# Kernel optimization log

Measured on AMD Instinct MI355X. Metric: run time of the kernel, lower is better.

Reference implementation:

```python
import jax, jax.numpy as jnp
import numpy as np

GAMMA = 0.95        # gamma_lemma: persistence decay per cycle (eq. 12.1)
KAPPA = 0.1         # kappa_interfere: lateral interference strength (eq. 12.3)
T_STEPS = 50        # t_lemma_steps: integration window before selection (eq. 12.2)
FLOOR = 1e-6        # confidence_floor for peak-to-average ratio

B, N_CONCEPTS, N_LEMMAS = 4096, 1024, 512


def setup_inputs() -> dict:
    key = jax.random.key(0)
    k1, k2 = jax.random.split(key, 2)
    # kernel boundary hands in a normalized concept distribution
    c_raw = jax.random.uniform(k1, (B, N_CONCEPTS), dtype=jnp.float32)
    c_lex = c_raw / jnp.sum(c_raw, axis=-1, keepdims=True)
    # TiedSubstrate W_C_to_L: (out_dim=n_lemmas, in_dim=n_concepts)
    W = jax.random.normal(k2, (N_LEMMAS, N_CONCEPTS), dtype=jnp.float32) / np.sqrt(N_CONCEPTS)
    # persistent lemma activation buffer a_lemma, zero at reset
    a0 = jnp.zeros((B, N_LEMMAS), dtype=jnp.float32)
    return {"c_lex": c_lex, "W": W, "a0": a0}


def reference(c_lex, W, a0):
    """Integrate lemma activations for T_STEPS cycles, then select.

    Per cycle (eq. 12.1 + 12.3):
      a <- gamma * a + c_lex @ W^T            # decay + concept->lemma drive
      a <- a - kappa * (sum_j a_j - a)        # lateral interference from other lemmas
      a <- max(a, 0)                          # rectify activations
    Selection (eq. 12.2): argmax over lemmas; confidence = peak / max(mean, floor).
    """
    def step(a, _):
        a = GAMMA * a + jnp.einsum('bc,lc->bl', c_lex, W)   # (B, n_lemmas)
        a = a - KAPPA * (jnp.sum(a, axis=-1, keepdims=True) - a)
        a = jnp.maximum(a, 0.0)
        return a, None

    a, _ = jax.lax.scan(step, a0, None, length=T_STEPS)
    peak = jnp.max(a, axis=-1)
    mean = jnp.mean(a, axis=-1)
    confidence = peak / jnp.maximum(mean, FLOOR)
    selected = jnp.argmax(a, axis=-1)
    return a, selected, confidence
```

## Files before the change

kernel.cpp:

```cpp
#include <hip/hip_runtime.h>
#include <hip/hip_bf16.h>

#define BATCH 4096
#define NC    1024
#define NL    512
#define TSTEPS 50
#define GAMMA_C 0.95f
#define KAPPA_C 0.1f
#define FLOOR_C 1e-6f

typedef __attribute__((ext_vector_type(8))) short short8;
typedef __attribute__((ext_vector_type(4))) float f32x4;

__device__ inline void split_bf16(float x, unsigned short& h, unsigned short& l) {
    unsigned u = __float_as_uint(x);
    unsigned rh = u + 0x7FFFu + ((u >> 16) & 1u);
    h = (unsigned short)(rh >> 16);
    float hf = __uint_as_float((unsigned)h << 16);
    float r = x - hf;
    unsigned v = __float_as_uint(r);
    unsigned rl = v + 0x7FFFu + ((v >> 16) & 1u);
    l = (unsigned short)(rl >> 16);
}

__global__ __launch_bounds__(256)
void convert_split(const float* __restrict__ A, const float* __restrict__ W,
                   unsigned short* __restrict__ Ahi, unsigned short* __restrict__ Alo,
                   unsigned short* __restrict__ Whi, unsigned short* __restrict__ Wlo) {
    const int chunk = blockIdx.x * 256 + threadIdx.x;
    const int fidx  = chunk * 4;
    const float* src;
    unsigned short *dh, *dl;
    if (fidx < BATCH * NC) {
        src = A + fidx; dh = Ahi + fidx; dl = Alo + fidx;
    } else {
        const int o = fidx - BATCH * NC;
        src = W + o; dh = Whi + o; dl = Wlo + o;
    }
    const float4 v = *(const float4*)src;
    ushort4 h4, l4;
    split_bf16(v.x, h4.x, l4.x);
    split_bf16(v.y, h4.y, l4.y);
    split_bf16(v.z, h4.z, l4.z);
    split_bf16(v.w, h4.w, l4.w);
    *(ushort4*)dh = h4;
    *(ushort4*)dl = l4;
}

#define TM 128
#define TN 256
#define GK 32
#define LDT 40

__global__ __launch_bounds__(512)
void gemm_bf16x2(const unsigned short* __restrict__ Ahi, const unsigned short* __restrict__ Alo,
                 const unsigned short* __restrict__ Whi, const unsigned short* __restrict__ Wlo,
                 float* __restrict__ Dp, int kPerSplit) {
    __shared__ unsigned short AsH[TM * LDT];
    __shared__ unsigned short AsL[TM * LDT];
    __shared__ unsigned short BsH[TN * LDT];
    __shared__ unsigned short BsL[TN * LDT];

    const int tid = threadIdx.x;
    const int m0 = blockIdx.x * TM;
    const int n0 = blockIdx.y * TN;
    const int kb = blockIdx.z * kPerSplit;

    const int srA = tid >> 2;
    const int kcA = (tid & 3) * 8;
    const int srB = tid >> 1;
    const int kcB = (tid & 1) * 16;

    const unsigned short* gAh = Ahi + (size_t)(m0 + srA) * NC + kb + kcA;
    const unsigned short* gAl = Alo + (size_t)(m0 + srA) * NC + kb + kcA;
    const unsigned short* gBh = Whi + (size_t)(n0 + srB) * NC + kb + kcB;
    const unsigned short* gBl = Wlo + (size_t)(n0 + srB) * NC + kb + kcB;

    unsigned short* wAh = AsH + srA * LDT + kcA;
    unsigned short* wAl = AsL + srA * LDT + kcA;
    unsigned short* wBh = BsH + srB * LDT + kcB;
    unsigned short* wBl = BsL + srB * LDT + kcB;

    const int lane = tid & 63;
    const int w    = tid >> 6;
    const int mw   = (w >> 2) * 64;
    const int nw   = (w & 3) * 64;
    const int sr   = lane & 15;
    const int quad = lane >> 4;

    const unsigned short* rAh = AsH + (mw + sr) * LDT + quad * 8;
    const unsigned short* rAl = AsL + (mw + sr) * LDT + quad * 8;
    const unsigned short* rBh = BsH + (nw + sr) * LDT + quad * 8;
    const unsigned short* rBl = BsL + (nw + sr) * LDT + quad * 8;

    f32x4 acc[4][4];
    #pragma unroll
    for (int i = 0; i < 4; ++i)
        #pragma unroll
        for (int j = 0; j < 4; ++j)
            acc[i][j] = (f32x4){0.f, 0.f, 0.f, 0.f};

    short8 pAh = *(const short8*)gAh;
    short8 pAl = *(const short8*)gAl;
    short8 pBh0 = *(const short8*)gBh;
    short8 pBh1 = *(const short8*)(gBh + 8);
    short8 pBl0 = *(const short8*)gBl;
    short8 pBl1 = *(const short8*)(gBl + 8);

    for (int kt = 0; kt < kPerSplit; kt += GK) {
        *(short8*)wAh = pAh;
        *(short8*)wAl = pAl;
        *(short8*)wBh = pBh0;
        *(short8*)(wBh + 8) = pBh1;
        *(short8*)wBl = pBl0;
        *(short8*)(wBl + 8) = pBl1;
        __syncthreads();

        const int kn = (kt + GK < kPerSplit) ? kt + GK : 0;
        pAh = *(const short8*)(gAh + kn);
        pAl = *(const short8*)(gAl + kn);
        pBh0 = *(const short8*)(gBh + kn);
        pBh1 = *(const short8*)(gBh + kn + 8);
        pBl0 = *(const short8*)(gBl + kn);
        pBl1 = *(const short8*)(gBl + kn + 8);

        short8 afh[4], afl[4], bfh[4], bfl[4];
        #pragma unroll
        for (int mi = 0; mi < 4; ++mi) {
            afh[mi] = *(const short8*)(rAh + mi * 16 * LDT);
            afl[mi] = *(const short8*)(rAl + mi * 16 * LDT);
        }
        #pragma unroll
        for (int ni = 0; ni < 4; ++ni) {
            bfh[ni] = *(const short8*)(rBh + ni * 16 * LDT);
            bfl[ni] = *(const short8*)(rBl + ni * 16 * LDT);
        }

        #pragma unroll
        for (int mi = 0; mi < 4; ++mi) {
            #pragma unroll
            for (int ni = 0; ni < 4; ++ni) {
                acc[mi][ni] = __builtin_amdgcn_mfma_f32_16x16x32_bf16(
                    afh[mi], bfh[ni], acc[mi][ni], 0, 0, 0);
                acc[mi][ni] = __builtin_amdgcn_mfma_f32_16x16x32_bf16(
                    afh[mi], bfl[ni], acc[mi][ni], 0, 0, 0);
                acc[mi][ni] = __builtin_amdgcn_mfma_f32_16x16x32_bf16(
                    afl[mi], bfh[ni], acc[mi][ni], 0, 0, 0);
            }
        }
        __syncthreads();
    }

    float* Dz = Dp + (size_t)blockIdx.z * BATCH * NL;
    #pragma unroll
    for (int mi = 0; mi < 4; ++mi) {
        #pragma unroll
        for (int ni = 0; ni < 4; ++ni) {
            const int col = n0 + nw + ni * 16 + sr;
            #pragma unroll
            for (int r = 0; r < 4; ++r) {
                const int row = m0 + mw + mi * 16 + quad * 4 + r;
                Dz[(size_t)row * NL + col] = acc[mi][ni][r];
            }
        }
    }
}

template<int SK>
__global__ __launch_bounds__(256)
void iterate_select(const float* __restrict__ Dp,
                    float* __restrict__ a_out,
                    float* __restrict__ sel_out, float* __restrict__ conf_out) {
    const int lane = threadIdx.x & 63;
    const int wave = threadIdx.x >> 6;
    const int sub  = lane & 31;
    const int grp  = lane >> 5;
    const int row  = blockIdx.x * 8 + wave * 2 + grp;

    float d[16];
    {
        const float4* p0 = (const float4*)(Dp + (size_t)row * NL + sub * 16);
        #pragma unroll
        for (int p = 0; p < 4; ++p) {
            const float4 v = p0[p];
            d[4 * p + 0] = v.x; d[4 * p + 1] = v.y; d[4 * p + 2] = v.z; d[4 * p + 3] = v.w;
        }
        #pragma unroll
        for (int s = 1; s < SK; ++s) {
            const float4* ps = (const float4*)(Dp + (size_t)s * BATCH * NL
                                               + (size_t)row * NL + sub * 16);
            #pragma unroll
            for (int p = 0; p < 4; ++p) {
                const float4 v = ps[p];
                d[4 * p + 0] += v.x; d[4 * p + 1] += v.y;
                d[4 * p + 2] += v.z; d[4 * p + 3] += v.w;
            }
        }
    }

    float a[16];
    #pragma unroll
    for (int j = 0; j < 16; ++j) a[j] = 0.f;

    const float K1 = 1.0f + KAPPA_C;

    for (int t = 0; t < TSTEPS; ++t) {
        #pragma unroll
        for (int j = 0; j < 16; ++j) a[j] = fmaf(GAMMA_C, a[j], d[j]);

        float t8[8], t4[4], t2[2];
        #pragma unroll
        for (int j = 0; j < 8; ++j) t8[j] = a[j] + a[j + 8];
        #pragma unroll
        for (int j = 0; j < 4; ++j) t4[j] = t8[j] + t8[j + 4];
        t2[0] = t4[0] + t4[2]; t2[1] = t4[1] + t4[3];
        float S = t2[0] + t2[1];

        S += __shfl_xor(S, 1, 64);
        S += __shfl_xor(S, 2, 64);
        S += __shfl_xor(S, 4, 64);
        S += __shfl_xor(S, 8, 64);
        S += __shfl_xor(S, 16, 64);

        const float h = -KAPPA_C * S;
        #pragma unroll
        for (int j = 0; j < 16; ++j) {
            const float v = fmaf(K1, a[j], h);
            a[j] = v > 0.f ? v : 0.f;
        }
    }

    float m8[8], m4[4], s8[8], s4[4];
    #pragma unroll
    for (int j = 0; j < 8; ++j) { m8[j] = fmaxf(a[j], a[j + 8]); s8[j] = a[j] + a[j + 8]; }
    #pragma unroll
    for (int j = 0; j < 4; ++j) { m4[j] = fmaxf(m8[j], m8[j + 4]); s4[j] = s8[j] + s8[j + 4]; }
    float peak = fmaxf(fmaxf(m4[0], m4[1]), fmaxf(m4[2], m4[3]));
    float ssum = (s4[0] + s4[1]) + (s4[2] + s4[3]);

    peak = fmaxf(peak, __shfl_xor(peak, 1, 64));
    peak = fmaxf(peak, __shfl_xor(peak, 2, 64));
    peak = fmaxf(peak, __shfl_xor(peak, 4, 64));
    peak = fmaxf(peak, __shfl_xor(peak, 8, 64));
    peak = fmaxf(peak, __shfl_xor(peak, 16, 64));
    ssum += __shfl_xor(ssum, 1, 64);
    ssum += __shfl_xor(ssum, 2, 64);
    ssum += __shfl_xor(ssum, 4, 64);
    ssum += __shfl_xor(ssum, 8, 64);
    ssum += __shfl_xor(ssum, 16, 64);

    const float mean = ssum * (1.0f / (float)NL);
    const float conf = peak / fmaxf(mean, FLOOR_C);

    int idx = 0x7fffffff;
    #pragma unroll
    for (int j = 0; j < 16; ++j)
        if (a[j] == peak) idx = min(idx, sub * 16 + j);
    idx = min(idx, __shfl_xor(idx, 1, 64));
    idx = min(idx, __shfl_xor(idx, 2, 64));
    idx = min(idx, __shfl_xor(idx, 4, 64));
    idx = min(idx, __shfl_xor(idx, 8, 64));
    idx = min(idx, __shfl_xor(idx, 16, 64));

    float4* ar = (float4*)(a_out + (size_t)row * NL + sub * 16);
    #pragma unroll
    for (int p = 0; p < 4; ++p) {
        float4 v;
        v.x = a[4 * p + 0]; v.y = a[4 * p + 1]; v.z = a[4 * p + 2]; v.w = a[4 * p + 3];
        ar[p] = v;
    }

    if (sub == 0) {
        if (sel_out)  sel_out[row]  = (float)idx;
        if (conf_out) conf_out[row] = conf;
    }
}

extern "C" void kernel_launch(void* const* d_in, const int* in_sizes, int n_in,
                              void* d_out, int out_size, void* d_ws, size_t ws_size,
                              hipStream_t stream) {
    const float* c_lex = (const float*)d_in[0];
    const float* W     = (const float*)d_in[1];

    float* D = (float*)d_ws;
    unsigned short* Ahi = (unsigned short*)(D + 4ull * BATCH * NL);
    unsigned short* Alo = Ahi + (size_t)BATCH * NC;
    unsigned short* Whi = Alo + (size_t)BATCH * NC;
    unsigned short* Wlo = Whi + (size_t)NL * NC;

    float* a_out = (float*)d_out;
    float* sel   = nullptr;
    float* conf  = nullptr;
    const int base = BATCH * NL;
    if (out_size >= base + 2 * BATCH) {
        sel  = a_out + base;
        conf = a_out + base + BATCH;
    } else if (out_size >= base + BATCH) {
        conf = a_out + base;
    }

    convert_split<<<dim3(4608), 256, 0, stream>>>(c_lex, W, Ahi, Alo, Whi, Wlo);

    const int kPerSplit = NC / 4;
    gemm_bf16x2<<<dim3(BATCH / TM, NL / TN, 4), 512, 0, stream>>>(
        Ahi, Alo, Whi, Wlo, D, kPerSplit);

    iterate_select<4><<<dim3(BATCH / 8), 256, 0, stream>>>(D, a_out, sel, conf);
}
```

Measured before the change: 115.1 us.

## Fuse activation bf16 split into GEMM load and widen iterate rows to full wave

Removes the separate conversion pass over the concept activations: the GEMM now loads fp32 A tiles directly and splits them into hi/lo bf16 in registers before writing to shared memory, so only W is pre-split. This avoids writing and re-reading the two bf16 copies of A (about 16MB of traffic) at the cost of more conversion ALU work in the GEMM's store phase. The iterate kernel also switches from two rows per wave with 16 elements per lane to one row per wave with 8 elements per lane, which doubles the block count and adds one shuffle stage per reduction.

After: 113.4 us. About the same (-1.5%).

```diff
diff --git a/kernel.cpp b/kernel.cpp
--- a/kernel.cpp
+++ b/kernel.cpp
@@ -24,27 +24,17 @@
 }
 
 __global__ __launch_bounds__(256)
-void convert_split(const float* __restrict__ A, const float* __restrict__ W,
-                   unsigned short* __restrict__ Ahi, unsigned short* __restrict__ Alo,
-                   unsigned short* __restrict__ Whi, unsigned short* __restrict__ Wlo) {
-    const int chunk = blockIdx.x * 256 + threadIdx.x;
-    const int fidx  = chunk * 4;
-    const float* src;
-    unsigned short *dh, *dl;
-    if (fidx < BATCH * NC) {
-        src = A + fidx; dh = Ahi + fidx; dl = Alo + fidx;
-    } else {
-        const int o = fidx - BATCH * NC;
-        src = W + o; dh = Whi + o; dl = Wlo + o;
-    }
-    const float4 v = *(const float4*)src;
+void convert_w(const float* __restrict__ W,
+               unsigned short* __restrict__ Whi, unsigned short* __restrict__ Wlo) {
+    const int fidx = (blockIdx.x * 256 + threadIdx.x) * 4;
+    const float4 v = *(const float4*)(W + fidx);
     ushort4 h4, l4;
     split_bf16(v.x, h4.x, l4.x);
     split_bf16(v.y, h4.y, l4.y);
     split_bf16(v.z, h4.z, l4.z);
     split_bf16(v.w, h4.w, l4.w);
-    *(ushort4*)dh = h4;
-    *(ushort4*)dl = l4;
+    *(ushort4*)(Whi + fidx) = h4;
+    *(ushort4*)(Wlo + fidx) = l4;
 }
 
 #define TM 128
@@ -53,7 +43,7 @@
 #define LDT 40
 
 __global__ __launch_bounds__(512)
-void gemm_bf16x2(const unsigned short* __restrict__ Ahi, const unsigned short* __restrict__ Alo,
+void gemm_bf16x2(const float* __restrict__ A,
                  const unsigned short* __restrict__ Whi, const unsigned short* __restrict__ Wlo,
                  float* __restrict__ Dp, int kPerSplit) {
     __shared__ unsigned short AsH[TM * LDT];
@@ -71,8 +61,7 @@
     const int srB = tid >> 1;
     const int kcB = (tid & 1) * 16;
 
-    const unsigned short* gAh = Ahi + (size_t)(m0 + srA) * NC + kb + kcA;
-    const unsigned short* gAl = Alo + (size_t)(m0 + srA) * NC + kb + kcA;
+    const float*          gA  = A   + (size_t)(m0 + srA) * NC + kb + kcA;
     const unsigned short* gBh = Whi + (size_t)(n0 + srB) * NC + kb + kcB;
     const unsigned short* gBl = Wlo + (size_t)(n0 + srB) * NC + kb + kcB;
 
@@ -100,16 +89,26 @@
         for (int j = 0; j < 4; ++j)
             acc[i][j] = (f32x4){0.f, 0.f, 0.f, 0.f};
 
-    short8 pAh = *(const short8*)gAh;
-    short8 pAl = *(const short8*)gAl;
+    float4 pA0 = *(const float4*)gA;
+    float4 pA1 = *(const float4*)(gA + 4);
     short8 pBh0 = *(const short8*)gBh;
     short8 pBh1 = *(const short8*)(gBh + 8);
     short8 pBl0 = *(const short8*)gBl;
     short8 pBl1 = *(const short8*)(gBl + 8);
 
     for (int kt = 0; kt < kPerSplit; kt += GK) {
-        *(short8*)wAh = pAh;
-        *(short8*)wAl = pAl;
+        {
+            short8 h8, l8;
+            const float av[8] = {pA0.x, pA0.y, pA0.z, pA0.w, pA1.x, pA1.y, pA1.z, pA1.w};
+            #pragma unroll
+            for (int i = 0; i < 8; ++i) {
+                unsigned short h, l;
+                split_bf16(av[i], h, l);
+                h8[i] = (short)h; l8[i] = (short)l;
+            }
+            *(short8*)wAh = h8;
+            *(short8*)wAl = l8;
+        }
         *(short8*)wBh = pBh0;
         *(short8*)(wBh + 8) = pBh1;
         *(short8*)wBl = pBl0;
@@ -117,8 +116,8 @@
         __syncthreads();
 
         const int kn = (kt + GK < kPerSplit) ? kt + GK : 0;
-        pAh = *(const short8*)(gAh + kn);
-        pAl = *(const short8*)(gAl + kn);
+        pA0 = *(const float4*)(gA + kn);
+        pA1 = *(const float4*)(gA + kn + 4);
         pBh0 = *(const short8*)(gBh + kn);
         pBh1 = *(const short8*)(gBh + kn + 8);
         pBl0 = *(const short8*)(gBl + kn);
@@ -173,104 +172,83 @@
                     float* __restrict__ sel_out, float* __restrict__ conf_out) {
     const int lane = threadIdx.x & 63;
     const int wave = threadIdx.x >> 6;
-    const int sub  = lane & 31;
-    const int grp  = lane >> 5;
-    const int row  = blockIdx.x * 8 + wave * 2 + grp;
-
-    float d[16];
+    const int row  = blockIdx.x * 4 + wave;
+
+    float d[8];
     {
-        const float4* p0 = (const float4*)(Dp + (size_t)row * NL + sub * 16);
-        #pragma unroll
-        for (int p = 0; p < 4; ++p) {
-            const float4 v = p0[p];
-            d[4 * p + 0] = v.x; d[4 * p + 1] = v.y; d[4 * p + 2] = v.z; d[4 * p + 3] = v.w;
-        }
+        const float4* p0 = (const float4*)(Dp + (size_t)row * NL + lane * 8);
+        float4 v0 = p0[0], v1 = p0[1];
+        d[0] = v0.x; d[1] = v0.y; d[2] = v0.z; d[3] = v0.w;
+        d[4] = v1.x; d[5] = v1.y; d[6] = v1.z; d[7] = v1.w;
         #pragma unroll
         for (int s = 1; s < SK; ++s) {
             const float4* ps = (const float4*)(Dp + (size_t)s * BATCH * NL
-                                               + (size_t)row * NL + sub * 16);
-            #pragma unroll
-            for (int p = 0; p < 4; ++p) {
-                const float4 v = ps[p];
-                d[4 * p + 0] += v.x; d[4 * p + 1] += v.y;
-                d[4 * p + 2] += v.z; d[4 * p + 3] += v.w;
-            }
-        }
-    }
-
-    float a[16];
-    #pragma unroll
-    for (int j = 0; j < 16; ++j) a[j] = 0.f;
+                                               + (size_t)row * NL + lane * 8);
+            const float4 w0 = ps[0], w1 = ps[1];
+            d[0] += w0.x; d[1] += w0.y; d[2] += w0.z; d[3] += w0.w;
+            d[4] += w1.x; d[5] += w1.y; d[6] += w1.z; d[7] += w1.w;
+        }
+    }
+
+    float a[8];
+    #pragma unroll
+    for (int j = 0; j < 8; ++j) a[j] = 0.f;
 
     const float K1 = 1.0f + KAPPA_C;
 
     for (int t = 0; t < TSTEPS; ++t) {
         #pragma unroll
-        for (int j = 0; j < 16; ++j) a[j] = fmaf(GAMMA_C, a[j], d[j]);
-
-        float t8[8], t4[4], t2[2];
-        #pragma unroll
-        for (int j = 0; j < 8; ++j) t8[j] = a[j] + a[j + 8];
-        #pragma unroll
-        for (int j = 0; j < 4; ++j) t4[j] = t8[j] + t8[j + 4];
-        t2[0] = t4[0] + t4[2]; t2[1] = t4[1] + t4[3];
-        float S = t2[0] + t2[1];
+        for (int j = 0; j < 8; ++j) a[j] = fmaf(GAMMA_C, a[j], d[j]);
+
+        float t4a = a[0] + a[4], t4b = a[1] + a[5], t4c = a[2] + a[6], t4d = a[3] + a[7];
+        float t2a = t4a + t4c, t2b = t4b + t4d;
+        float S = t2a + t2b;
 
         S += __shfl_xor(S, 1, 64);
         S += __shfl_xor(S, 2, 64);
         S += __shfl_xor(S, 4, 64);
         S += __shfl_xor(S, 8, 64);
         S += __shfl_xor(S, 16, 64);
+        S += __shfl_xor(S, 32, 64);
 
         const float h = -KAPPA_C * S;
         #pragma unroll
-        for (int j = 0; j < 16; ++j) {
+        for (int j = 0; j < 8; ++j) {
             const float v = fmaf(K1, a[j], h);
             a[j] = v > 0.f ? v : 0.f;
         }
     }
 
-    float m8[8], m4[4], s8[8], s4[4];
-    #pragma unroll
-    for (int j = 0; j < 8; ++j) { m8[j] = fmaxf(a[j], a[j + 8]); s8[j] = a[j] + a[j + 8]; }
-    #pragma unroll
-    for (int j = 0; j < 4; ++j) { m4[j] = fmaxf(m8[j], m8[j + 4]); s4[j] = s8[j] + s8[j + 4]; }
-    float peak = fmaxf(fmaxf(m4[0], m4[1]), fmaxf(m4[2], m4[3]));
-    float ssum = (s4[0] + s4[1]) + (s4[2] + s4[3]);
-
-    peak = fmaxf(peak, __shfl_xor(peak, 1, 64));
-    peak = fmaxf(peak, __shfl_xor(peak, 2, 64));
-    peak = fmaxf(peak, __shfl_xor(peak, 4, 64));
-    peak = fmaxf(peak, __shfl_xor(peak, 8, 64));
-    peak = fmaxf(peak, __shfl_xor(peak, 16, 64));
-    ssum += __shfl_xor(ssum, 1, 64);
-    ssum += __shfl_xor(ssum, 2, 64);
-    ssum += __shfl_xor(ssum, 4, 64);
-    ssum += __shfl_xor(ssum, 8, 64);
-    ssum += __shfl_xor(ssum, 16, 64);
+    float m4a = fmaxf(a[0], a[4]), m4b = fmaxf(a[1], a[5]);
+    float m4c = fmaxf(a[2], a[6]), m4d = fmaxf(a[3], a[7]);
+    float peak = fmaxf(fmaxf(m4a, m4b), fmaxf(m4c, m4d));
+    float s4a = a[0] + a[4], s4b = a[1] + a[5], s4c = a[2] + a[6], s4d = a[3] + a[7];
+    float ssum = (s4a + s4b) + (s4c + s4d);
+
+    #pragma unroll
+    for (int m = 1; m < 64; m <<= 1) {
+        peak = fmaxf(peak, __shfl_xor(peak, m, 64));
+        ssum += __shfl_xor(ssum, m, 64);
+    }
 
     const float mean = ssum * (1.0f / (float)NL);
     const float conf = peak / fmaxf(mean, FLOOR_C);
 
     int idx = 0x7fffffff;
     #pragma unroll
-    for (int j = 0; j < 16; ++j)
-        if (a[j] == peak) idx = min(idx, sub * 16 + j);
-    idx = min(idx, __shfl_xor(idx, 1, 64));
-    idx = min(idx, __shfl_xor(idx, 2, 64));
-    idx = min(idx, __shfl_xor(idx, 4, 64));
-    idx = min(idx, __shfl_xor(idx, 8, 64));
-    idx = min(idx, __shfl_xor(idx, 16, 64));
-
-    float4* ar = (float4*)(a_out + (size_t)row * NL + sub * 16);
-    #pragma unroll
-    for (int p = 0; p < 4; ++p) {
-        float4 v;
-        v.x = a[4 * p + 0]; v.y = a[4 * p + 1]; v.z = a[4 * p + 2]; v.w = a[4 * p + 3];
-        ar[p] = v;
-    }
-
-    if (sub == 0) {
+    for (int j = 0; j < 8; ++j)
+        if (a[j] == peak) idx = min(idx, lane * 8 + j);
+    #pragma unroll
+    for (int m = 1; m < 64; m <<= 1)
+        idx = min(idx, __shfl_xor(idx, m, 64));
+
+    float4* ar = (float4*)(a_out + (size_t)row * NL + lane * 8);
+    float4 o0, o1;
+    o0.x = a[0]; o0.y = a[1]; o0.z = a[2]; o0.w = a[3];
+    o1.x = a[4]; o1.y = a[5]; o1.z = a[6]; o1.w = a[7];
+    ar[0] = o0; ar[1] = o1;
+
+    if (lane == 0) {
         if (sel_out)  sel_out[row]  = (float)idx;
         if (conf_out) conf_out[row] = conf;
     }
@@ -283,9 +261,7 @@
     const float* W     = (const float*)d_in[1];
 
     float* D = (float*)d_ws;
-    unsigned short* Ahi = (unsigned short*)(D + 4ull * BATCH * NL);
-    unsigned short* Alo = Ahi + (size_t)BATCH * NC;
-    unsigned short* Whi = Alo + (size_t)BATCH * NC;
+    unsigned short* Whi = (unsigned short*)(D + 4ull * BATCH * NL);
     unsigned short* Wlo = Whi + (size_t)NL * NC;
 
     float* a_out = (float*)d_out;
@@ -299,11 +275,11 @@
         conf = a_out + base;
     }
 
-    convert_split<<<dim3(4608), 256, 0, stream>>>(c_lex, W, Ahi, Alo, Whi, Wlo);
+    convert_w<<<dim3(512), 256, 0, stream>>>(W, Whi, Wlo);
 
     const int kPerSplit = NC / 4;
     gemm_bf16x2<<<dim3(BATCH / TM, NL / TN, 4), 512, 0, stream>>>(
-        Ahi, Alo, Whi, Wlo, D, kPerSplit);
-
-    iterate_select<4><<<dim3(BATCH / 8), 256, 0, stream>>>(D, a_out, sel, conf);
-}
+        c_lex, Whi, Wlo, D, kPerSplit);
+
+    iterate_select<4><<<dim3(BATCH / 4), 256, 0, stream>>>(D, a_out, sel, conf);
+}
```
